# Kernel tuning notes

Measured on AMD Instinct MI355X. Metric: run time of the kernel, lower is better.

## Reference

```python
import jax, jax.numpy as jnp
import numpy as np

H, C = 33, 16  # heads, out_channels (concat=False -> mean over heads)
NEG_SLOPE = 0.2


def setup_inputs() -> dict:
    key = jax.random.key(0)
    ks = jax.random.split(key, 6)
    N, E, F_in = 50000, 320000, 128
    x = jax.random.normal(ks[0], (N, F_in), dtype=jnp.float32)
    edge_index = jax.random.randint(ks[1], (2, E), 0, N, dtype=jnp.int64)
    W = jax.random.normal(ks[2], (F_in, H * C), dtype=jnp.float32) * (1.0 / np.sqrt(F_in))
    att_src = jax.random.normal(ks[3], (H, C), dtype=jnp.float32) * 0.1
    att_dst = jax.random.normal(ks[4], (H, C), dtype=jnp.float32) * 0.1
    bias = jnp.zeros((C,), dtype=jnp.float32)
    return {"x": x, "edge_index": edge_index, "W": W, "att_src": att_src, "att_dst": att_dst, "bias": bias}


def reference(x, edge_index, W, att_src, att_dst, bias):
    N = x.shape[0]
    # add self loops (PyG GATConv default add_self_loops=True)
    loop = jnp.arange(N, dtype=edge_index.dtype)
    src = jnp.concatenate([edge_index[0], loop])  # [Et]
    dst = jnp.concatenate([edge_index[1], loop])  # [Et]

    h = (x @ W).reshape(N, H, C)                       # [N,H,C]
    a_src = jnp.einsum('nhc,hc->nh', h, att_src)       # [N,H]
    a_dst = jnp.einsum('nhc,hc->nh', h, att_dst)       # [N,H]

    e = a_src[src] + a_dst[dst]                        # [Et,H]
    e = jnp.where(e > 0, e, NEG_SLOPE * e)             # leaky_relu

    # segment softmax over incoming edges of each destination node
    m = jax.ops.segment_max(e, dst, num_segments=N)    # [N,H]
    ex = jnp.exp(e - m[dst])                           # [Et,H]
    denom = jax.ops.segment_sum(ex, dst, num_segments=N)  # [N,H]
    alpha = ex / (denom[dst] + 1e-16)                  # [Et,H]

    msg = alpha[:, :, None] * h[src]                   # [Et,H,C]
    out = jax.ops.segment_sum(msg, dst, num_segments=N)  # [N,H,C]
    out = out.mean(axis=1) + bias                      # concat=False -> mean heads
    return jnp.tanh(out)
```

## Files before the change

### kernel.cpp

```cpp
#include <hip/hip_runtime.h>
#include <math.h>

#define H_HEADS 33
#define C_CH    16
#define HC      528
#define JG      11
#define JGT     13
#define F_IN    128
#define NEG_SLOPE 0.2f

#define BSH   7
#define BMAX  1024
#define PCH   4096

typedef short  bf16x8  __attribute__((ext_vector_type(8)));
typedef float  floatx4 __attribute__((ext_vector_type(4)));
typedef float  floatx2 __attribute__((ext_vector_type(2)));

__device__ inline unsigned short f2bf(float f) {
    unsigned int u = __float_as_uint(f);
    unsigned int r = u + 0x7fffu + ((u >> 16) & 1u);
    return (unsigned short)(r >> 16);
}
__device__ inline float bflo(unsigned int u) {
    return __uint_as_float(u << 16);
}
__device__ inline float bfhi(unsigned int u) {
    return __uint_as_float(u & 0xffff0000u);
}

__device__ inline void load_edges4(const int* __restrict__ ei, int E, int Et,
                                   int e0, int* src, int* dst)
{
    if (e0 + 3 < E) {
        int4 s4 = *(const int4*)&ei[e0];
        src[0] = s4.x; src[1] = s4.y; src[2] = s4.z; src[3] = s4.w;
        if ((E & 3) == 0) {
            int4 d4 = *(const int4*)&ei[E + e0];
            dst[0] = d4.x; dst[1] = d4.y; dst[2] = d4.z; dst[3] = d4.w;
        } else {
            #pragma unroll
            for (int k = 0; k < 4; ++k) dst[k] = ei[E + e0 + k];
        }
    } else {
        #pragma unroll
        for (int k = 0; k < 4; ++k) {
            int g = e0 + k;
            if (g < E)       { src[k] = ei[g]; dst[k] = ei[E + g]; }
            else if (g < Et) { src[k] = dst[k] = g - E; }
            else             { src[k] = dst[k] = -1; }
        }
    }
}

#define PW1 (F_IN * HC)
#define PW2 (PW1 + 96 * F_IN)
__global__ void prep_kernel(const float* __restrict__ W,
                            const float* __restrict__ att_src,
                            const float* __restrict__ att_dst,
                            unsigned short* __restrict__ Wt,
                            float4* __restrict__ zout, int nzo)
{
    int g = blockIdx.x * blockDim.x + threadIdx.x;
    if (g < PW1) {
        int k = g / HC, n = g % HC;
        Wt[n * F_IN + k] = f2bf(W[g]);
    } else if (g < PW2) {
        int gg = g - PW1;
        int nl = gg >> 7, k = gg & 127;
        int grp = nl / 48, h = nl % 48;
        float v = 0.f;
        if (h < H_HEADS) {
            const float* att = grp ? att_dst : att_src;
            const float* wr  = W + (size_t)k * HC + h * C_CH;
            #pragma unroll
            for (int c = 0; c < C_CH; ++c) v += wr[c] * att[h * C_CH + c];
        }
        Wt[(size_t)(HC + nl) * F_IN + k] = f2bf(v);
    } else {
        int z = g - PW2;
        if (z < nzo) zout[z] = make_float4(0.f, 0.f, 0.f, 0.f);
    }
}

#define LDA 136
__global__ __launch_bounds__(256) void gemm_att_kernel(
    const float* __restrict__ x, const unsigned short* __restrict__ Wt,
    unsigned short* __restrict__ hb,
    float* __restrict__ a_src, float* __restrict__ a_dstc, int N)
{
    __shared__ unsigned short U[64 * LDA];
    unsigned short (*As)[LDA] = (unsigned short (*)[LDA])U;
    unsigned short (*Bs)[LDA] = (unsigned short (*)[LDA])U;

    const int tid  = threadIdx.x;
    const int lane = tid & 63;
    const int wave = tid >> 6;
    const int lm   = lane & 15;
    const int kc   = lane >> 4;
    const int m0   = blockIdx.x * 64;
    const size_t segN = (size_t)N * 48;

    for (int e = tid; e < 64 * 32; e += 256) {
        int r = e >> 5, c = e & 31;
        int gr = m0 + r;
        float4 v = (gr < N) ? ((const float4*)(x + (size_t)gr * F_IN))[c]
                            : make_float4(0.f, 0.f, 0.f, 0.f);
        unsigned int lo = (unsigned int)f2bf(v.x) | ((unsigned int)f2bf(v.y) << 16);
        unsigned int hi = (unsigned int)f2bf(v.z) | ((unsigned int)f2bf(v.w) << 16);
        *(uint2*)&As[r][c * 4] = make_uint2(lo, hi);
    }

    const uint4* wp = (const uint4*)Wt;
    uint4 rb0 = wp[tid], rb1 = wp[tid + 256], rb2 = wp[tid + 512];

    __syncthreads();

    const int arow = wave * 16 + lm;
    bf16x8 afrag[4];
    #pragma unroll
    for (int ks = 0; ks < 4; ++ks)
        afrag[ks] = *(const bf16x8*)&As[arow][ks * 32 + kc * 8];

    #pragma unroll 1
    for (int j = 0; j < JGT; ++j) {
        __syncthreads();
        *(uint4*)&Bs[tid >> 4][(tid & 15) * 8] = rb0;
        { int e = tid + 256; *(uint4*)&Bs[e >> 4][(e & 15) * 8] = rb1; }
        { int e = tid + 512; *(uint4*)&Bs[e >> 4][(e & 15) * 8] = rb2; }
        if (j + 1 < JGT) {
            int b = (j + 1) * 768;
            rb0 = wp[b + tid]; rb1 = wp[b + tid + 256]; rb2 = wp[b + tid + 512];
        }
        __syncthreads();

        floatx4 acc[3] = {};
        #pragma unroll
        for (int ks = 0; ks < 4; ++ks) {
            #pragma unroll
            for (int t = 0; t < 3; ++t) {
                bf16x8 b = *(const bf16x8*)&Bs[t * 16 + lm][ks * 32 + kc * 8];
                acc[t] = __builtin_amdgcn_mfma_f32_16x16x32_bf16(afrag[ks], b, acc[t], 0, 0, 0);
            }
        }

        #pragma unroll
        for (int t = 0; t < 3; ++t) {
            #pragma unroll
            for (int rr = 0; rr < 4; ++rr) {
                const int row = m0 + wave * 16 + kc * 4 + rr;
                if (row >= N) continue;
                if (j < JG) {
                    hb[(size_t)j * segN + (size_t)row * 48 + t * 16 + lm] =
                        f2bf(acc[t][rr]);
                } else {
                    const int col = t * 16 + lm;
                    if (col < H_HEADS) {
                        float* dstp = (j == JG) ? a_src : a_dstc;
                        dstp[(size_t)row * H_HEADS + col] = acc[t][rr];
                    }
                }
            }
        }
    }
}

__global__ __launch_bounds__(256) void bhist_kernel(const int* __restrict__ ei,
                                                    int* __restrict__ bhist,
                                                    int E, int Et)
{
    __shared__ int lh[2 * BMAX];
    const int tid = threadIdx.x;
    for (int i = tid; i < 2 * BMAX; i += 256) lh[i] = 0;
    __syncthreads();
    int e0 = (blockIdx.x * 256 + tid) * 8;
    if (e0 < Et) {
        int s4[4], d4[4];
        #pragma unroll
        for (int h = 0; h < 2; ++h) {
            load_edges4(ei, E, Et, e0 + h * 4, s4, d4);
            #pragma unroll
            for (int k = 0; k < 4; ++k)
                if (s4[k] >= 0) {
                    atomicAdd(&lh[s4[k] >> BSH], 1);
                    atomicAdd(&lh[BMAX + (d4[k] >> BSH)], 1);
                }
        }
    }
    __syncthreads();
    for (int i = tid; i < 2 * BMAX; i += 256) {
        int v = lh[i];
        if (v) atomicAdd(&bhist[i], v);
    }
}

__global__ __launch_bounds__(1024) void scanb_kernel(const int* __restrict__ bhist,
                                                     int* __restrict__ bbase,
                                                     int* __restrict__ cursor,
                                                     int nb)
{
    const int side = blockIdx.x;
    const int tid  = threadIdx.x;
    const int* h = bhist + side * BMAX;
    int* bb  = bbase  + side * (BMAX + 1);
    int* cur = cursor + side * BMAX;
    __shared__ int sa[1024];
    int v = (tid < nb) ? h[tid] : 0;
    sa[tid] = v;
    __syncthreads();
    for (int off = 1; off < 1024; off <<= 1) {
        int t = (tid >= off) ? sa[tid - off] : 0;
        __syncthreads();
        sa[tid] += t;
        __syncthreads();
    }
    int incl = sa[tid];
    if (tid < nb) {
        bb[tid]  = incl - v;
        cur[tid] = incl - v;
        if (tid == nb - 1) bb[nb] = incl;
    }
}

__global__ __launch_bounds__(256) void part_kernel(const int* __restrict__ ei,
                                                   int* __restrict__ cursor,
                                                   int2* __restrict__ Ag,
                                                   int E, int Et)
{
    __shared__ int2 kv[PCH];
    __shared__ int  lhist[512];
    __shared__ int  gbias[512];
    __shared__ int  wsum[4];
    __shared__ int  sTot;

    const int side = blockIdx.y;
    const int tid  = threadIdx.x;
    const int lane = tid & 63, wid = tid >> 6;
    for (int i = tid; i < 512; i += 256) lhist[i] = 0;
    __syncthreads();

    const int c0 = blockIdx.x * PCH;
    int2 kvr[16];
    #pragma unroll
    for (int r = 0; r < 4; ++r) {
        int e0 = c0 + r * 1024 + tid * 4;
        int s4[4], d4[4];
        load_edges4(ei, E, Et, e0, s4, d4);
        #pragma unroll
        for (int k = 0; k < 4; ++k) {
            int key = side ? d4[k] : s4[k];
            int val = side ? s4[k] : d4[k];
            kvr[r * 4 + k] = make_int2(key, val);
            if (key >= 0) atomicAdd(&lhist[key >> BSH], 1);
        }
    }
    __syncthreads();

    int a0 = lhist[2 * tid], a1 = lhist[2 * tid + 1];
    int pair = a0 + a1, s = pair;
    #pragma unroll
    for (int d = 1; d < 64; d <<= 1) {
        int t = __shfl_up(s, d);
        if (lane >= d) s += t;
    }
    if (lane == 63) wsum[wid] = s;
    __syncthreads();
    if (tid == 0) {
        int run = 0;
        #pragma unroll
        for (int i = 0; i < 4; ++i) { int t = wsum[i]; wsum[i] = run; run += t; }
    }
    __syncthreads();
    int exclT = s - pair + wsum[wid];
    int e0x = exclT, e1x = exclT + a0;
    if (tid == 255) sTot = e1x + a1;
    lhist[2 * tid]     = e0x;
    lhist[2 * tid + 1] = e1x;
    if (a0 > 0) {
        int gb = atomicAdd(&cursor[side * BMAX + 2 * tid], a0);
        gbias[2 * tid] = gb - e0x;
    }
    if (a1 > 0) {
        int gb = atomicAdd(&cursor[side * BMAX + 2 * tid + 1], a1);
        gbias[2 * tid + 1] = gb - e1x;
    }
    __syncthreads();

    #pragma unroll
    for (int k = 0; k < 16; ++k) {
        int key = kvr[k].x;
        if (key >= 0) {
            int lp = atomicAdd(&lhist[key >> BSH], 1);
            kv[lp] = kvr[k];
        }
    }
    __syncthreads();

    const int tot = sTot;
    for (int i = tid; i < tot; i += 256) {
        int2 e = kv[i];
        int b = e.x >> BSH;
        Ag[(size_t)side * Et + gbias[b] + i] = e;
    }
}

__global__ __launch_bounds__(256) void p2_kernel(const int2* __restrict__ Ag,
                                                 const int* __restrict__ bbase,
                                                 int2* __restrict__ e2,
                                                 int* __restrict__ ss2,
                                                 int* __restrict__ off_d,
                                                 int N, int Et, int nb)
{
    const int side = blockIdx.y;
    const int b    = blockIdx.x;
    if (b >= nb) return;
    const int tid  = threadIdx.x;
    const int base = bbase[side * (BMAX + 1) + b];
    const int end  = bbase[side * (BMAX + 1) + b + 1];
    const int k0   = b << BSH;
    const int2* A  = Ag + (size_t)side * Et;

    __shared__ int lh[128];
    __shared__ int w0s;
    if (tid < 128) lh[tid] = 0;
    __syncthreads();
    for (int i = base + tid; i < end; i += 256)
        atomicAdd(&lh[A[i].x - k0], 1);
    __syncthreads();

    int v = 0, s = 0;
    if (tid < 128) {
        v = lh[tid]; s = v;
        #pragma unroll
        for (int d = 1; d < 64; d <<= 1) {
            int t = __shfl_up(s, d);
            if ((tid & 63) >= d) s += t;
        }
    }
    if (tid == 63) w0s = s;
    __syncthreads();
    if (tid >= 64 && tid < 128) s += w0s;
    int start = base + s - v;
    if (tid < 128) {
        lh[tid] = start;
        if (side == 1 && (k0 + tid) < N) off_d[k0 + tid] = start;
    }
    __syncthreads();

    for (int i = base + tid; i < end; i += 256) {
        int2 e = A[i];
        int pos = atomicAdd(&lh[e.x - k0], 1);
        if (side == 0) e2[pos] = e;
        else           ss2[pos] = e.y;
    }
}

__global__ __launch_bounds__(256) void denom_kernel(
    const int* __restrict__ off_d, const int* __restrict__ ss2,
    const float* __restrict__ a_src, const float* __restrict__ a_dstc,
    float* __restrict__ ad2, int N, int Et)
{
    int g = blockIdx.x * blockDim.x + threadIdx.x;
    if (g >= N * H_HEADS) return;
    const int d = g / H_HEADS, h = g - d * H_HEADS;
    const int beg = off_d[d];
    const int end = (d + 1 < N) ? off_d[d + 1] : Et;
    const float ad = a_dstc[g];
    float acc = 0.f;
    int e = beg;
    for (; e + 4 <= end; e += 4) {
        int s0 = ss2[e], s1 = ss2[e + 1], s2 = ss2[e + 2], s3 = ss2[e + 3];
        float v0 = a_src[(size_t)s0 * H_HEADS + h];
        float v1 = a_src[(size_t)s1 * H_HEADS + h];
        float v2 = a_src[(size_t)s2 * H_HEADS + h];
        float v3 = a_src[(size_t)s3 * H_HEADS + h];
        v0 += ad; v0 = v0 > 0.f ? v0 : NEG_SLOPE * v0;
        v1 += ad; v1 = v1 > 0.f ? v1 : NEG_SLOPE * v1;
        v2 += ad; v2 = v2 > 0.f ? v2 : NEG_SLOPE * v2;
        v3 += ad; v3 = v3 > 0.f ? v3 : NEG_SLOPE * v3;
        acc += __expf(v0); acc += __expf(v1);
        acc += __expf(v2); acc += __expf(v3);
    }
    for (; e < end; ++e) {
        float v = a_src[(size_t)ss2[e] * H_HEADS + h] + ad;
        v = v > 0.f ? v : NEG_SLOPE * v;
        acc += __expf(v);
    }
    ((float2*)ad2)[g] = make_float2(ad, 1.0f / (acc + 1e-16f));
}

#define EPB  64
#define RCAP 20
#define RSTR 536
__global__ __launch_bounds__(256, 4) void aggregate_kernel(
    const int2* __restrict__ e2,
    const float* __restrict__ a_src, const float* __restrict__ ad2,
    const unsigned short* __restrict__ hb,
    float* __restrict__ out, int N, int Et)
{
    __shared__ int   s_src[EPB], s_dst[EPB];
    __shared__ float s_alpha[EPB][H_HEADS];
    __shared__ int   s_ridx[EPB];
    __shared__ int   s_rowsrc[RCAP];
    __shared__ int   s_U;
    __shared__ __align__(16) unsigned short Hrow[RCAP * RSTR];

    const int nwg = gridDim.x;
    const int q = nwg >> 3, r = nwg & 7;
    const int xcd = blockIdx.x & 7, idx = blockIdx.x >> 3;
    const int bid = (xcd < r ? xcd * (q + 1) : r * (q + 1) + (xcd - r) * q) + idx;

    const int tid = threadIdx.x;
    const int e0  = bid * EPB;
    const size_t segN = (size_t)N * 48;

    if (tid < EPB) {
        int e = e0 + tid;
        int2 v = (e < Et) ? e2[e] : make_int2(0, 0);
        s_src[tid] = v.x; s_dst[tid] = v.y;
    }
    __syncthreads();

    if (tid < 64) {
        int src = s_src[tid];
        bool flag = (tid == 0) || (src != s_src[tid - 1]);
        unsigned long long b = __ballot(flag);
        int cntb = __popcll(b & ((1ull << tid) - 1));
        int run  = flag ? cntb : cntb - 1;
        s_ridx[tid] = (run < RCAP) ? run : -1;
        if (flag && run < RCAP) s_rowsrc[run] = src;
        if (tid == 63) s_U = __popcll(b);
    }
    __syncthreads();

    int Un = s_U; if (Un > RCAP) Un = RCAP;
    for (int i = tid; i < Un * 66; i += 256) {
        int rr = i / 66, c = i - rr * 66;
        int j = c / 6, qq = c - j * 6;
        int srcr = s_rowsrc[rr];
        uint4 v = *(const uint4*)(hb + (size_t)j * segN + (size_t)srcr * 48 + qq * 8);
        *(uint4*)&Hrow[rr * RSTR + j * 48 + qq * 8] = v;
    }

    float2 di[9]; float as[9];
    #pragma unroll
    for (int rr = 0; rr < 8; ++rr) {
        int i = tid + rr * 256;
        int el = i / H_HEADS, hd = i - el * H_HEADS;
        di[rr] = ((const float2*)ad2)[(size_t)s_dst[el] * H_HEADS + hd];
        as[rr] = a_src[(size_t)s_src[el] * H_HEADS + hd];
    }
    if (tid < 64) {
        int i = 2048 + tid;
        int el = i / H_HEADS, hd = i - el * H_HEADS;
        di[8] = ((const float2*)ad2)[(size_t)s_dst[el] * H_HEADS + hd];
        as[8] = a_src[(size_t)s_src[el] * H_HEADS + hd];
    }
    __builtin_amdgcn_sched_barrier(0);
    #pragma unroll
    for (int rr = 0; rr < 8; ++rr) {
        int i = tid + rr * 256;
        int el = i / H_HEADS, hd = i - el * H_HEADS;
        float v = as[rr] + di[rr].x;
        v = v > 0.f ? v : NEG_SLOPE * v;
        s_alpha[el][hd] = __expf(v) * di[rr].y;
    }
    if (tid < 64) {
        int i = 2048 + tid;
        int el = i / H_HEADS, hd = i - el * H_HEADS;
        float v = as[8] + di[8].x;
        v = v > 0.f ? v : NEG_SLOPE * v;
        s_alpha[el][hd] = __expf(v) * di[8].y;
    }
    __syncthreads();

    const int el = tid >> 2, cq = tid & 3;
    const int rid = s_ridx[el];
    floatx2 acc01 = {0.f, 0.f}, acc23 = {0.f, 0.f};
    if (rid >= 0) {
        const unsigned short* pr = &Hrow[rid * RSTR + cq * 4];
        #pragma unroll
        for (int j = 0; j < JG; ++j) {
            uint2 wA = *(const uint2*)(pr + j * 48);
            uint2 wB = *(const uint2*)(pr + j * 48 + 16);
            uint2 wC = *(const uint2*)(pr + j * 48 + 32);
            float l0 = s_alpha[el][3 * j + 0];
            float l1 = s_alpha[el][3 * j + 1];
            float l2 = s_alpha[el][3 * j + 2];
            floatx2 hA0 = {bflo(wA.x), bfhi(wA.x)};
            floatx2 hB0 = {bflo(wB.x), bfhi(wB.x)};
            floatx2 hC0 = {bflo(wC.x), bfhi(wC.x)};
            floatx2 hA1 = {bflo(wA.y), bfhi(wA.y)};
            floatx2 hB1 = {bflo(wB.y), bfhi(wB.y)};
            floatx2 hC1 = {bflo(wC.y), bfhi(wC.y)};
            acc01 += hA0 * l0 + hB0 * l1 + hC0 * l2;
            acc23 += hA1 * l0 + hB1 * l1 + hC1 * l2;
        }
    } else {
        const unsigned short* hp = hb + (size_t)s_src[el] * 48 + cq * 4;
        #pragma unroll
        for (int j = 0; j < JG; ++j) {
            const unsigned short* pj = hp + (size_t)j * segN;
            uint2 wA = *(const uint2*)(pj);
            uint2 wB = *(const uint2*)(pj + 16);
            uint2 wC = *(const uint2*)(pj + 32);
            float l0 = s_alpha[el][3 * j + 0];
            float l1 = s_alpha[el][3 * j + 1];
            float l2 = s_alpha[el][3 * j + 2];
            floatx2 hA0 = {bflo(wA.x), bfhi(wA.x)};
            floatx2 hB0 = {bflo(wB.x), bfhi(wB.x)};
            floatx2 hC0 = {bflo(wC.x), bfhi(wC.x)};
            floatx2 hA1 = {bflo(wA.y), bfhi(wA.y)};
            floatx2 hB1 = {bflo(wB.y), bfhi(wB.y)};
            floatx2 hC1 = {bflo(wC.y), bfhi(wC.y)};
            acc01 += hA0 * l0 + hB0 * l1 + hC0 * l2;
            acc23 += hA1 * l0 + hB1 * l1 + hC1 * l2;
        }
    }
    float a0 = acc01.x, a1 = acc01.y, a2 = acc23.x, a3 = acc23.y;

    const int lane  = tid & 63;
    const int wbase = (tid >> 6) * 16;
    #pragma unroll
    for (int qx = 0; qx < 4; ++qx) {
        int S = 16 * qx + ((lane >> 4) << 2) + ((lane & 15) >> 2);
        float s0 = __shfl(a0, S), s1 = __shfl(a1, S);
        float s2 = __shfl(a2, S), s3 = __shfl(a3, S);
        float v = (lane & 2) ? ((lane & 1) ? s3 : s2)
                             : ((lane & 1) ? s1 : s0);
        int elT = wbase + qx * 4 + (lane >> 4);
        if (e0 + elT < Et)
            atomicAdd(&out[s_dst[elT] * C_CH + (lane & 15)], v);
    }
}

__global__ void finalize_kernel(float* __restrict__ out,
                                const float* __restrict__ bias, int total)
{
    int g = blockIdx.x * blockDim.x + threadIdx.x;
    if (g >= total) return;
    out[g] = tanhf(out[g] * (1.0f / 33.0f) + bias[g & 15]);
}

extern "C" void kernel_launch(void* const* d_in, const int* in_sizes, int n_in,
                              void* d_out, int out_size, void* d_ws, size_t ws_size,
                              hipStream_t stream)
{
    const float* x       = (const float*)d_in[0];
    const int*   ei      = (const int*)  d_in[1];
    const float* W       = (const float*)d_in[2];
    const float* att_src = (const float*)d_in[3];
    const float* att_dst = (const float*)d_in[4];
    const float* bias    = (const float*)d_in[5];
    float* out = (float*)d_out;

    const int N  = in_sizes[0] / F_IN;
    const int E  = in_sizes[1] / 2;
    const int Et = E + N;
    const int nb = (N + 127) >> BSH;

    unsigned short* hb = (unsigned short*)d_ws;
    float* a_src  = (float*)(hb + (size_t)N * HC);
    float* a_dstc = a_src + (size_t)N * H_HEADS;
    float* ad2    = a_dstc + (size_t)N * H_HEADS;
    int2*  e2     = (int2*)(ad2 + (size_t)N * 66);
    int*   ss2    = (int*)(e2 + Et);
    int*   off_d  = ss2 + Et;
    int2*  Ag     = (int2*)(off_d + N);
    int*   bhist  = (int*)(Ag + 2 * (size_t)Et);
    int*   bbase  = bhist + 2 * BMAX;
    int*   cursor = bbase + 2 * (BMAX + 1);
    unsigned short* Wt = (unsigned short*)(cursor + 2 * BMAX);

    hipMemsetAsync(bhist, 0, 2 * BMAX * sizeof(int), stream);

    const int nzo = out_size / 4;
    const int prepTot = PW2 + nzo;
    prep_kernel<<<(prepTot + 255) / 256, 256, 0, stream>>>(
        W, att_src, att_dst, Wt, (float4*)out, nzo);

    gemm_att_kernel<<<(N + 63) / 64, 256, 0, stream>>>(x, Wt, hb, a_src, a_dstc, N);

    bhist_kernel<<<(Et + 2047) / 2048, 256, 0, stream>>>(ei, bhist, E, Et);
    scanb_kernel<<<2, 1024, 0, stream>>>(bhist, bbase, cursor, nb);
    part_kernel<<<dim3((Et + PCH - 1) / PCH, 2), 256, 0, stream>>>(
        ei, cursor, Ag, E, Et);
    p2_kernel<<<dim3(nb, 2), 256, 0, stream>>>(Ag, bbase, e2, ss2, off_d,
                                               N, Et, nb);

    denom_kernel<<<(N * H_HEADS + 255) / 256, 256, 0, stream>>>(
        off_d, ss2, a_src, a_dstc, ad2, N, Et);

    aggregate_kernel<<<(Et + EPB - 1) / EPB, 256, 0, stream>>>(
        e2, a_src, ad2, hb, out, N, Et);

    int totO = N * C_CH;
    finalize_kernel<<<(totO + 255) / 256, 256, 0, stream>>>(out, bias, totO);
}
```

Measured before the change: 188.8 us.

## Fuse edge histogram into prep kernel and split GEMM column groups across grid

The bucket histogram work moves into extra blocks of the prep kernel, which removes one kernel launch and lets the histogram run alongside the weight transpose. The GEMM kernel gains a second grid dimension that splits its 13 column groups 7/6 between two blocks per row tile, doubling block count for more parallelism. The cost is that each of the two blocks converts and loads the same x tile, and the prep kernel now reserves 8KB of shared memory in every block, including blocks that never use it.

```diff
diff --git a/kernel.cpp b/kernel.cpp
--- a/kernel.cpp
+++ b/kernel.cpp
@@ -59,9 +59,40 @@
                             const float* __restrict__ att_src,
                             const float* __restrict__ att_dst,
                             unsigned short* __restrict__ Wt,
-                            float4* __restrict__ zout, int nzo)
-{
-    int g = blockIdx.x * blockDim.x + threadIdx.x;
+                            float4* __restrict__ zout, int nzo,
+                            const int* __restrict__ ei,
+                            int* __restrict__ bhist, int E, int Et,
+                            int prepBlocks)
+{
+    __shared__ int lh[2 * BMAX];
+    const int tid = threadIdx.x;
+
+    if (blockIdx.x >= prepBlocks) {
+        for (int i = tid; i < 2 * BMAX; i += 256) lh[i] = 0;
+        __syncthreads();
+        int e0 = ((blockIdx.x - prepBlocks) * 256 + tid) * 8;
+        if (e0 < Et) {
+            int s4[4], d4[4];
+            #pragma unroll
+            for (int h = 0; h < 2; ++h) {
+                load_edges4(ei, E, Et, e0 + h * 4, s4, d4);
+                #pragma unroll
+                for (int k = 0; k < 4; ++k)
+                    if (s4[k] >= 0) {
+                        atomicAdd(&lh[s4[k] >> BSH], 1);
+                        atomicAdd(&lh[BMAX + (d4[k] >> BSH)], 1);
+                    }
+            }
+        }
+        __syncthreads();
+        for (int i = tid; i < 2 * BMAX; i += 256) {
+            int v = lh[i];
+            if (v) atomicAdd(&bhist[i], v);
+        }
+        return;
+    }
+
+    int g = blockIdx.x * blockDim.x + tid;
     if (g < PW1) {
         int k = g / HC, n = g % HC;
         Wt[n * F_IN + k] = f2bf(W[g]);
@@ -99,6 +130,8 @@
     const int lm   = lane & 15;
     const int kc   = lane >> 4;
     const int m0   = blockIdx.x * 64;
+    const int jbeg = blockIdx.y ? 7 : 0;
+    const int jend = blockIdx.y ? JGT : 7;
     const size_t segN = (size_t)N * 48;
 
     for (int e = tid; e < 64 * 32; e += 256) {
@@ -112,7 +145,9 @@
     }
 
     const uint4* wp = (const uint4*)Wt;
-    uint4 rb0 = wp[tid], rb1 = wp[tid + 256], rb2 = wp[tid + 512];
+    uint4 rb0 = wp[jbeg * 768 + tid];
+    uint4 rb1 = wp[jbeg * 768 + tid + 256];
+    uint4 rb2 = wp[jbeg * 768 + tid + 512];
 
     __syncthreads();
 
@@ -123,12 +158,12 @@
         afrag[ks] = *(const bf16x8*)&As[arow][ks * 32 + kc * 8];
 
     #pragma unroll 1
-    for (int j = 0; j < JGT; ++j) {
+    for (int j = jbeg; j < jend; ++j) {
         __syncthreads();
         *(uint4*)&Bs[tid >> 4][(tid & 15) * 8] = rb0;
         { int e = tid + 256; *(uint4*)&Bs[e >> 4][(e & 15) * 8] = rb1; }
         { int e = tid + 512; *(uint4*)&Bs[e >> 4][(e & 15) * 8] = rb2; }
-        if (j + 1 < JGT) {
+        if (j + 1 < jend) {
             int b = (j + 1) * 768;
             rb0 = wp[b + tid]; rb1 = wp[b + tid + 256]; rb2 = wp[b + tid + 512];
         }
@@ -162,35 +197,6 @@
                 }
             }
         }
-    }
-}
-
-__global__ __launch_bounds__(256) void bhist_kernel(const int* __restrict__ ei,
-                                                    int* __restrict__ bhist,
-                                                    int E, int Et)
-{
-    __shared__ int lh[2 * BMAX];
-    const int tid = threadIdx.x;
-    for (int i = tid; i < 2 * BMAX; i += 256) lh[i] = 0;
-    __syncthreads();
-    int e0 = (blockIdx.x * 256 + tid) * 8;
-    if (e0 < Et) {
-        int s4[4], d4[4];
-        #pragma unroll
-        for (int h = 0; h < 2; ++h) {
-            load_edges4(ei, E, Et, e0 + h * 4, s4, d4);
-            #pragma unroll
-            for (int k = 0; k < 4; ++k)
-                if (s4[k] >= 0) {
-                    atomicAdd(&lh[s4[k] >> BSH], 1);
-                    atomicAdd(&lh[BMAX + (d4[k] >> BSH)], 1);
-                }
-        }
-    }
-    __syncthreads();
-    for (int i = tid; i < 2 * BMAX; i += 256) {
-        int v = lh[i];
-        if (v) atomicAdd(&bhist[i], v);
     }
 }
 
@@ -575,13 +581,14 @@
     hipMemsetAsync(bhist, 0, 2 * BMAX * sizeof(int), stream);
 
     const int nzo = out_size / 4;
-    const int prepTot = PW2 + nzo;
-    prep_kernel<<<(prepTot + 255) / 256, 256, 0, stream>>>(
-        W, att_src, att_dst, Wt, (float4*)out, nzo);
-
-    gemm_att_kernel<<<(N + 63) / 64, 256, 0, stream>>>(x, Wt, hb, a_src, a_dstc, N);
-
-    bhist_kernel<<<(Et + 2047) / 2048, 256, 0, stream>>>(ei, bhist, E, Et);
+    const int prepBlocks  = (PW2 + nzo + 255) / 256;
+    const int bhistBlocks = (Et + 2047) / 2048;
+    prep_kernel<<<prepBlocks + bhistBlocks, 256, 0, stream>>>(
+        W, att_src, att_dst, Wt, (float4*)out, nzo, ei, bhist, E, Et, prepBlocks);
+
+    gemm_att_kernel<<<dim3((N + 63) / 64, 2), 256, 0, stream>>>(
+        x, Wt, hb, a_src, a_dstc, N);
+
     scanb_kernel<<<2, 1024, 0, stream>>>(bhist, bbase, cursor, nb);
     part_kernel<<<dim3((Et + PCH - 1) / PCH, 2), 256, 0, stream>>>(
         ei, cursor, Ag, E, Et);
```

Result: no change. 189.5 us (+0.4%).
